# Optimization experiments

Hardware: AMD Instinct MI355X
Metric: run time of the kernel (lower is better)

Reference implementation:

```python
import jax, jax.numpy as jnp
import numpy as np

BUFFER_C = 1.25

def setup_inputs() -> dict:
    key = jax.random.key(0)
    k1, k2, k3 = jax.random.split(key, 3)
    T, D, E = 4096, 1024, 8
    x = jax.random.normal(k1, (T, D), dtype=jnp.float32)
    Wg = jax.random.normal(k2, (D, E), dtype=jnp.float32) / np.sqrt(D)
    bg = jnp.zeros((E,), dtype=jnp.float32)
    W = jax.random.normal(k3, (E, D, D), dtype=jnp.float32) / np.sqrt(D)
    b = jnp.zeros((E, D), dtype=jnp.float32)
    return {"x": x, "Wg": Wg, "bg": bg, "W": W, "b": b}


def reference(x, Wg, bg, W, b):
    # Top-1 (Switch-style) routing with capacity buffer, per-expert Linear,
    # prob-weighted combine, plus load-balancing aux loss.
    T, D = x.shape
    E = W.shape[0]
    capacity = int(BUFFER_C * T / E)

    logits = x @ Wg + bg                      # [T, E]
    probs = jax.nn.softmax(logits, axis=-1)   # [T, E]
    top_idx = jnp.argmax(probs, axis=-1)      # [T]
    top_prob = jnp.take_along_axis(probs, top_idx[:, None], axis=-1)[:, 0]

    onehot = jax.nn.one_hot(top_idx, E, dtype=x.dtype)       # [T, E]
    # 1-indexed position of each token within its expert's buffer
    pos = jnp.cumsum(onehot, axis=0) * onehot                # [T, E]
    dispatch = jnp.where((onehot > 0) & (pos <= capacity), 1.0, 0.0).astype(x.dtype)

    # dense dispatch/combine equivalent of the masked per-expert loop
    xe = jnp.einsum('te,td->etd', dispatch, x)               # [E, T, D]
    ye = jnp.einsum('etd,edf->etf', xe, W) + b[:, None, :]   # [E, T, D]
    y = jnp.einsum('te,etf->tf', dispatch, ye)               # [T, D] (0 for dropped)
    out = y * top_prob[:, None]

    # aux load-balance loss: E * sum_e f_e * P_e
    f = onehot.mean(axis=0)
    P = probs.mean(axis=0)
    aux_loss = E * jnp.sum(f * P)
    return out, aux_loss
```

## Files before the change

### kernel.cpp

```cpp
#include <hip/hip_runtime.h>
#include <hip/hip_bf16.h>
#include <cstdint>

#define T_TOK 4096
#define D_DIM 1024
#define E_EXP 8
#define CAP   640
#define NBIN  64
#define MAXDROP 3456
#define MT    10

typedef __attribute__((ext_vector_type(8))) short short8;
typedef __attribute__((ext_vector_type(4))) float f32x4;

__device__ inline unsigned short f2bf(float f) {
    uint32_t u = __float_as_uint(f);
    u += 0x7fffu + ((u >> 16) & 1u);
    return (unsigned short)(u >> 16);
}

__device__ inline void dma16(const void* g, void* l) {
    __builtin_amdgcn_global_load_lds(
        (const __attribute__((address_space(1))) unsigned int*)g,
        (__attribute__((address_space(3))) unsigned int*)l, 16, 0, 0);
}

#define WB_TILE(e, nt, kt) ((((size_t)(e) * 16 + (nt)) * 16 + (kt)) * 4096)
#define XG_TILE(e, mt, kt) ((((size_t)(e) * MT + (mt)) * 16 + (kt)) * 4096)

__global__ __launch_bounds__(256) void prep_kernel(
    const float* __restrict__ x, const float* __restrict__ Wg,
    const float* __restrict__ bg, const float* __restrict__ W,
    unsigned short* __restrict__ Wb,
    int* __restrict__ top_idx, float* __restrict__ top_prob, float* __restrict__ ppart)
{
    int bid = blockIdx.x;
    int tid = threadIdx.x;

    if (bid < 2048) {
        __shared__ unsigned short tile[64][66];
        int e  = bid >> 8;
        int kt = (bid >> 4) & 15;
        int nt = bid & 15;
        int k0 = kt * 64, n0 = nt * 64;
        const float* Wsrc = W + (size_t)e * D_DIM * D_DIM;
        #pragma unroll
        for (int p = 0; p < 4; p++) {
            int kk = p * 16 + (tid >> 4);
            int nn = (tid & 15) * 4;
            float4 v = *(const float4*)(Wsrc + (size_t)(k0 + kk) * D_DIM + n0 + nn);
            ushort4 u;
            u.x = f2bf(v.x); u.y = f2bf(v.y); u.z = f2bf(v.z); u.w = f2bf(v.w);
            *(ushort4*)&tile[kk][nn] = u;
        }
        __syncthreads();
        unsigned short* dst = Wb + WB_TILE(e, nt, kt);
        #pragma unroll
        for (int p = 0; p < 2; p++) {
            int c = tid + 256 * p;
            int g = c >> 6, n = c & 63;
            short8 v;
            #pragma unroll
            for (int z = 0; z < 8; z++) v[z] = (short)tile[g * 8 + z][n];
            *(short8*)&dst[(size_t)c * 8] = v;
        }
    } else {
        int wid  = tid >> 6;
        int lane = tid & 63;
        int t = (bid - 2048) * 4 + wid;

        const float* xr = x + (size_t)t * D_DIM;

        float acc[8];
        #pragma unroll
        for (int e = 0; e < 8; e++) acc[e] = 0.f;

        #pragma unroll
        for (int ii = 0; ii < 16; ii++) {
            int d = lane + 64 * ii;
            float xv = xr[d];
            const float4* wr = (const float4*)(Wg + (size_t)d * 8);
            float4 a = wr[0], bq = wr[1];
            acc[0] += xv * a.x;  acc[1] += xv * a.y;
            acc[2] += xv * a.z;  acc[3] += xv * a.w;
            acc[4] += xv * bq.x; acc[5] += xv * bq.y;
            acc[6] += xv * bq.z; acc[7] += xv * bq.w;
        }
        #pragma unroll
        for (int off = 32; off > 0; off >>= 1) {
            #pragma unroll
            for (int e = 0; e < 8; e++) acc[e] += __shfl_xor(acc[e], off, 64);
        }
        if (lane == 0) {
            float lg[8];
            #pragma unroll
            for (int e = 0; e < 8; e++) lg[e] = acc[e] + bg[e];
            float m = lg[0]; int am = 0;
            #pragma unroll
            for (int e = 1; e < 8; e++) { if (lg[e] > m) { m = lg[e]; am = e; } }
            float ex[8], s = 0.f;
            #pragma unroll
            for (int e = 0; e < 8; e++) { ex[e] = expf(lg[e] - m); s += ex[e]; }
            float inv = 1.f / s;
            top_idx[t]  = am;
            top_prob[t] = ex[am] * inv;
            int bin = (int)(bid & (NBIN - 1));
            #pragma unroll
            for (int e = 0; e < 8; e++) atomicAdd(&ppart[bin * 8 + e], ex[e] * inv);
        }
    }
}

__global__ __launch_bounds__(1024) void scan_kernel(
    const int* __restrict__ top_idx,
    int* __restrict__ tok_list, int* __restrict__ cnt,
    const float* __restrict__ ppart,
    float* __restrict__ out, float* __restrict__ out_aux)
{
    __shared__ int counts[64][8];
    __shared__ int excl[64][8];
    __shared__ int fulltot[8];
    __shared__ int droplist[MAXDROP];
    __shared__ int ndrop;

    int tid  = threadIdx.x;
    int wv   = tid >> 6;
    int lane = tid & 63;
    unsigned long long ltmask = (lane == 0) ? 0ull : ((~0ull) >> (64 - lane));

    if (tid == 0) ndrop = 0;

    int ecache[4];
    #pragma unroll
    for (int c = 0; c < 4; c++)
        ecache[c] = top_idx[(4 * wv + c) * 64 + lane];

    #pragma unroll
    for (int c = 0; c < 4; c++) {
        int chunk = 4 * wv + c;
        int e = ecache[c];
        #pragma unroll
        for (int q = 0; q < 8; q++) {
            unsigned long long mk = __ballot(e == q);
            int tot = __popcll(mk);
            if (lane == q) counts[chunk][q] = tot;
        }
    }
    __syncthreads();

    if (wv == 0) {
        #pragma unroll
        for (int q = 0; q < 8; q++) {
            int v = counts[lane][q];
            int orig = v;
            #pragma unroll
            for (int off = 1; off < 64; off <<= 1) {
                int n = __shfl_up(v, off, 64);
                if (lane >= off) v += n;
            }
            excl[lane][q] = v - orig;
            int total = __shfl(v, 63, 64);
            if (lane == 0) {
                fulltot[q] = total;
                cnt[q] = total < CAP ? total : CAP;
            }
        }
    }
    __syncthreads();

    #pragma unroll
    for (int c = 0; c < 4; c++) {
        int chunk = 4 * wv + c;
        int t = chunk * 64 + lane;
        int e = ecache[c];
        int pos = 0;
        #pragma unroll
        for (int q = 0; q < 8; q++) {
            unsigned long long mk = __ballot(e == q);
            if (e == q) pos = excl[chunk][q] + __popcll(mk & ltmask);
        }
        if (pos < CAP) {
            tok_list[e * CAP + pos] = t;
        } else {
            int di = atomicAdd(&ndrop, 1);
            droplist[di] = t;
        }
    }
    __syncthreads();

    int nd = ndrop;
    int grp = tid >> 8;
    int col = (tid & 255) * 4;
    float4 z = {0.f, 0.f, 0.f, 0.f};
    for (int d = grp; d < nd; d += 4) {
        int row = droplist[d];
        *(float4*)&out[(size_t)row * D_DIM + col] = z;
    }

    if (wv == 0) {
        float p[8];
        #pragma unroll
        for (int e = 0; e < 8; e++) p[e] = ppart[lane * 8 + e];
        #pragma unroll
        for (int off = 32; off > 0; off >>= 1) {
            #pragma unroll
            for (int e = 0; e < 8; e++) p[e] += __shfl_xor(p[e], off, 64);
        }
        if (lane == 0) {
            float s = 0.f;
            #pragma unroll
            for (int e = 0; e < 8; e++)
                s += ((float)fulltot[e] / (float)T_TOK) * (p[e] / (float)T_TOK);
            out_aux[0] = (float)E_EXP * s;
        }
    }
}

__global__ __launch_bounds__(256) void gather_kernel(
    const float* __restrict__ x, const int* __restrict__ tok_list,
    const int* __restrict__ cnt, unsigned short* __restrict__ xg)
{
    int bid = blockIdx.x;
    int e   = bid / 40;
    int rem = bid % 40;
    int mt  = rem >> 2, ktg = rem & 3;
    int count = cnt[e];
    int m0 = mt * 64;
    if (m0 >= count) return;

    int tid = threadIdx.x;
    const int* tl = tok_list + e * CAP;

    #pragma unroll
    for (int kk = 0; kk < 4; kk++) {
        int kt = ktg * 4 + kk;
        unsigned short* dst = xg + XG_TILE(e, mt, kt);
        #pragma unroll
        for (int p = 0; p < 2; p++) {
            int c = tid + 256 * p;
            int g = c >> 6, row = c & 63;
            int gm = m0 + row;
            int tok = tl[gm < count ? gm : count - 1];
            const float* src = x + (size_t)tok * D_DIM + kt * 64 + g * 8;
            float4 v0 = *(const float4*)(src);
            float4 v1 = *(const float4*)(src + 4);
            short8 v;
            v[0] = f2bf(v0.x); v[1] = f2bf(v0.y); v[2] = f2bf(v0.z); v[3] = f2bf(v0.w);
            v[4] = f2bf(v1.x); v[5] = f2bf(v1.y); v[6] = f2bf(v1.z); v[7] = f2bf(v1.w);
            *(short8*)&dst[(size_t)c * 8] = v;
        }
    }
}

__device__ inline void stage_dma(const unsigned short* gAt, const unsigned short* gBt,
                                 unsigned short (*Ab)[64][8], unsigned short (*Bb)[64][8],
                                 int w, int lane)
{
    size_t lo = (size_t)lane * 8;
    dma16(gAt + (size_t)w * 512 + lo,       &Ab[w][0][0]);
    dma16(gAt + (size_t)(w + 4) * 512 + lo, &Ab[w + 4][0][0]);
    dma16(gBt + (size_t)w * 512 + lo,       &Bb[w][0][0]);
    dma16(gBt + (size_t)(w + 4) * 512 + lo, &Bb[w + 4][0][0]);
}

__global__ __launch_bounds__(256) void expert_gemm(
    const unsigned short* __restrict__ xg, const unsigned short* __restrict__ Wb,
    const float* __restrict__ bias,
    const int* __restrict__ tok_list, const int* __restrict__ cnt,
    const float* __restrict__ top_prob, float* __restrict__ out)
{
    int bid = blockIdx.x;
    int e   = bid / (MT * 16);
    int rem = bid % (MT * 16);
    int mt  = rem >> 4, nt = rem & 15;
    int count = cnt[e];
    int m0 = mt * 64;
    if (m0 >= count) return;
    int n0 = nt * 64;

    __shared__ unsigned short Ab[2][8][64][8];
    __shared__ unsigned short Bb[2][8][64][8];

    int tid  = threadIdx.x;
    int lane = tid & 63, w = tid >> 6;
    int quad = lane >> 4, l16 = lane & 15;
    int mw = (w >> 1) * 32, nw = (w & 1) * 32;

    const int* tl = tok_list + e * CAP;
    const unsigned short* gA0 = xg + XG_TILE(e, mt, 0);
    const unsigned short* gB0 = Wb + WB_TILE(e, nt, 0);

    f32x4 acc[2][2];
    #pragma unroll
    for (int i = 0; i < 2; i++)
        #pragma unroll
        for (int j = 0; j < 2; j++)
            acc[i][j] = (f32x4){0.f, 0.f, 0.f, 0.f};

    stage_dma(gA0, gB0, Ab[0], Bb[0], w, lane);

    int cur = 0;
    #pragma unroll 1
    for (int kt = 0; kt < 16; kt++) {
        __syncthreads();
        if (kt + 1 < 16)
            stage_dma(gA0 + (size_t)(kt + 1) * 4096, gB0 + (size_t)(kt + 1) * 4096,
                      Ab[cur ^ 1], Bb[cur ^ 1], w, lane);

        short8 af[2][2], bf[2][2];
        #pragma unroll
        for (int s = 0; s < 2; s++) {
            #pragma unroll
            for (int i = 0; i < 2; i++) {
                af[s][i] = *(const short8*)&Ab[cur][s * 4 + quad][mw + 16 * i + l16][0];
                bf[s][i] = *(const short8*)&Bb[cur][s * 4 + quad][nw + 16 * i + l16][0];
            }
        }
        #pragma unroll
        for (int s = 0; s < 2; s++)
            #pragma unroll
            for (int i = 0; i < 2; i++)
                #pragma unroll
                for (int j = 0; j < 2; j++)
                    acc[i][j] = __builtin_amdgcn_mfma_f32_16x16x32_bf16(
                        af[s][i], bf[s][j], acc[i][j], 0, 0, 0);
        cur ^= 1;
    }

    float bv[2];
    #pragma unroll
    for (int j = 0; j < 2; j++)
        bv[j] = bias[e * D_DIM + n0 + nw + 16 * j + l16];

    #pragma unroll
    for (int i = 0; i < 2; i++) {
        int rb = m0 + mw + 16 * i + quad * 4;
        #pragma unroll
        for (int r = 0; r < 4; r++) {
            int gm = rb + r;
            if (gm >= count) continue;
            int tok = tl[gm];
            float p = top_prob[tok];
            float* orow = out + (size_t)tok * D_DIM + n0 + nw + l16;
            #pragma unroll
            for (int j = 0; j < 2; j++)
                orow[16 * j] = (acc[i][j][r] + bv[j]) * p;
        }
    }
}

extern "C" void kernel_launch(void* const* d_in, const int* in_sizes, int n_in,
                              void* d_out, int out_size, void* d_ws, size_t ws_size,
                              hipStream_t stream) {
    const float* x  = (const float*)d_in[0];
    const float* Wg = (const float*)d_in[1];
    const float* bg = (const float*)d_in[2];
    const float* W  = (const float*)d_in[3];
    const float* b  = (const float*)d_in[4];
    float* out = (float*)d_out;

    char* ws = (char*)d_ws;
    unsigned short* Wb = (unsigned short*)(ws + 0);
    unsigned short* xg = (unsigned short*)(ws + 16777216);
    int*   top_idx  = (int*)(ws + 27262976);
    float* top_prob = (float*)(ws + 27279360);
    int*   tok_list = (int*)(ws + 27295744);
    int*   cnt      = (int*)(ws + 27316224);
    float* ppart    = (float*)(ws + 27316256);

    hipMemsetAsync(ppart, 0, NBIN * 8 * sizeof(float), stream);
    hipLaunchKernelGGL(prep_kernel, dim3(2048 + T_TOK / 4), dim3(256), 0, stream,
                       x, Wg, bg, W, Wb, top_idx, top_prob, ppart);
    hipLaunchKernelGGL(scan_kernel, dim3(1), dim3(1024), 0, stream,
                       top_idx, tok_list, cnt, ppart, out, out + (size_t)T_TOK * D_DIM);
    hipLaunchKernelGGL(gather_kernel, dim3(320), dim3(256), 0, stream,
                       x, tok_list, cnt, xg);
    hipLaunchKernelGGL(expert_gemm, dim3(E_EXP * MT * 16), dim3(256), 0, stream,
                       xg, Wb, b, tok_list, cnt, top_prob, out);
}
```

Before: 170.2 us.

## Replace atomic prob accumulation with per-block partials and widen gather grid

The router blocks now write per-block probability sums through shared memory instead of doing global atomicAdds into binned accumulators, and the scan kernel reduces the 1024 partials across all its waves. This removes the memset launch and the atomic contention. The gating blocks are moved ahead of the weight-conversion blocks so routing finishes earlier. The gather kernel also uses one block per k-tile instead of four, giving 4x more blocks for better parallelism, and expf is swapped for __expf, which can slightly change the softmax values.

```diff
diff --git a/kernel.cpp b/kernel.cpp
--- a/kernel.cpp
+++ b/kernel.cpp
@@ -6,9 +6,9 @@
 #define D_DIM 1024
 #define E_EXP 8
 #define CAP   640
-#define NBIN  64
 #define MAXDROP 3456
 #define MT    10
+#define GBLK  1024
 
 typedef __attribute__((ext_vector_type(8))) short short8;
 typedef __attribute__((ext_vector_type(4))) float f32x4;
@@ -32,16 +32,18 @@
     const float* __restrict__ x, const float* __restrict__ Wg,
     const float* __restrict__ bg, const float* __restrict__ W,
     unsigned short* __restrict__ Wb,
-    int* __restrict__ top_idx, float* __restrict__ top_prob, float* __restrict__ ppart)
+    int* __restrict__ top_idx, float* __restrict__ top_prob,
+    float* __restrict__ blkpart)
 {
     int bid = blockIdx.x;
     int tid = threadIdx.x;
 
-    if (bid < 2048) {
+    if (bid >= GBLK) {
         __shared__ unsigned short tile[64][66];
-        int e  = bid >> 8;
-        int kt = (bid >> 4) & 15;
-        int nt = bid & 15;
+        int bid2 = bid - GBLK;
+        int e  = bid2 >> 8;
+        int kt = (bid2 >> 4) & 15;
+        int nt = bid2 & 15;
         int k0 = kt * 64, n0 = nt * 64;
         const float* Wsrc = W + (size_t)e * D_DIM * D_DIM;
         #pragma unroll
@@ -65,9 +67,10 @@
             *(short8*)&dst[(size_t)c * 8] = v;
         }
     } else {
+        __shared__ float probs_sm[4][8];
         int wid  = tid >> 6;
         int lane = tid & 63;
-        int t = (bid - 2048) * 4 + wid;
+        int t = bid * 4 + wid;
 
         const float* xr = x + (size_t)t * D_DIM;
 
@@ -100,13 +103,20 @@
             for (int e = 1; e < 8; e++) { if (lg[e] > m) { m = lg[e]; am = e; } }
             float ex[8], s = 0.f;
             #pragma unroll
-            for (int e = 0; e < 8; e++) { ex[e] = expf(lg[e] - m); s += ex[e]; }
+            for (int e = 0; e < 8; e++) { ex[e] = __expf(lg[e] - m); s += ex[e]; }
             float inv = 1.f / s;
             top_idx[t]  = am;
             top_prob[t] = ex[am] * inv;
-            int bin = (int)(bid & (NBIN - 1));
-            #pragma unroll
-            for (int e = 0; e < 8; e++) atomicAdd(&ppart[bin * 8 + e], ex[e] * inv);
+            #pragma unroll
+            for (int e = 0; e < 8; e++) probs_sm[wid][e] = 0.f;
+            #pragma unroll
+            for (int e = 0; e < 8; e++) probs_sm[wid][e] = ex[e] * inv;
+        }
+        __syncthreads();
+        if (tid < 8) {
+            float s = probs_sm[0][tid] + probs_sm[1][tid]
+                    + probs_sm[2][tid] + probs_sm[3][tid];
+            blkpart[(size_t)bid * 8 + tid] = s;
         }
     }
 }
@@ -114,7 +124,7 @@
 __global__ __launch_bounds__(1024) void scan_kernel(
     const int* __restrict__ top_idx,
     int* __restrict__ tok_list, int* __restrict__ cnt,
-    const float* __restrict__ ppart,
+    const float* __restrict__ blkpart,
     float* __restrict__ out, float* __restrict__ out_aux)
 {
     __shared__ int counts[64][8];
@@ -122,6 +132,7 @@
     __shared__ int fulltot[8];
     __shared__ int droplist[MAXDROP];
     __shared__ int ndrop;
+    __shared__ float wpart[16][8];
 
     int tid  = threadIdx.x;
     int wv   = tid >> 6;
@@ -129,6 +140,14 @@
     unsigned long long ltmask = (lane == 0) ? 0ull : ((~0ull) >> (64 - lane));
 
     if (tid == 0) ndrop = 0;
+
+    float p[8];
+    {
+        const float4* bp = (const float4*)(blkpart + (size_t)tid * 8);
+        float4 p0 = bp[0], p1 = bp[1];
+        p[0] = p0.x; p[1] = p0.y; p[2] = p0.z; p[3] = p0.w;
+        p[4] = p1.x; p[5] = p1.y; p[6] = p1.z; p[7] = p1.w;
+    }
 
     int ecache[4];
     #pragma unroll
@@ -186,6 +205,16 @@
             droplist[di] = t;
         }
     }
+
+    #pragma unroll
+    for (int off = 32; off > 0; off >>= 1) {
+        #pragma unroll
+        for (int e = 0; e < 8; e++) p[e] += __shfl_xor(p[e], off, 64);
+    }
+    if (lane == 0) {
+        #pragma unroll
+        for (int e = 0; e < 8; e++) wpart[wv][e] = p[e];
+    }
     __syncthreads();
 
     int nd = ndrop;
@@ -197,22 +226,16 @@
         *(float4*)&out[(size_t)row * D_DIM + col] = z;
     }
 
-    if (wv == 0) {
-        float p[8];
-        #pragma unroll
-        for (int e = 0; e < 8; e++) p[e] = ppart[lane * 8 + e];
-        #pragma unroll
-        for (int off = 32; off > 0; off >>= 1) {
-            #pragma unroll
-            for (int e = 0; e < 8; e++) p[e] += __shfl_xor(p[e], off, 64);
-        }
-        if (lane == 0) {
-            float s = 0.f;
-            #pragma unroll
-            for (int e = 0; e < 8; e++)
-                s += ((float)fulltot[e] / (float)T_TOK) * (p[e] / (float)T_TOK);
-            out_aux[0] = (float)E_EXP * s;
-        }
+    if (tid == 0) {
+        float s = 0.f;
+        #pragma unroll
+        for (int e = 0; e < 8; e++) {
+            float Pe = 0.f;
+            #pragma unroll
+            for (int w = 0; w < 16; w++) Pe += wpart[w][e];
+            s += ((float)fulltot[e] / (float)T_TOK) * (Pe / (float)T_TOK);
+        }
+        out_aux[0] = (float)E_EXP * s;
     }
 }
 
@@ -221,34 +244,30 @@
     const int* __restrict__ cnt, unsigned short* __restrict__ xg)
 {
     int bid = blockIdx.x;
-    int e   = bid / 40;
-    int rem = bid % 40;
-    int mt  = rem >> 2, ktg = rem & 3;
+    int e   = bid / (MT * 16);
+    int rem = bid % (MT * 16);
+    int mt  = rem >> 4, kt = rem & 15;
     int count = cnt[e];
     int m0 = mt * 64;
     if (m0 >= count) return;
 
     int tid = threadIdx.x;
     const int* tl = tok_list + e * CAP;
-
-    #pragma unroll
-    for (int kk = 0; kk < 4; kk++) {
-        int kt = ktg * 4 + kk;
-        unsigned short* dst = xg + XG_TILE(e, mt, kt);
-        #pragma unroll
-        for (int p = 0; p < 2; p++) {
-            int c = tid + 256 * p;
-            int g = c >> 6, row = c & 63;
-            int gm = m0 + row;
-            int tok = tl[gm < count ? gm : count - 1];
-            const float* src = x + (size_t)tok * D_DIM + kt * 64 + g * 8;
-            float4 v0 = *(const float4*)(src);
-            float4 v1 = *(const float4*)(src + 4);
-            short8 v;
-            v[0] = f2bf(v0.x); v[1] = f2bf(v0.y); v[2] = f2bf(v0.z); v[3] = f2bf(v0.w);
-            v[4] = f2bf(v1.x); v[5] = f2bf(v1.y); v[6] = f2bf(v1.z); v[7] = f2bf(v1.w);
-            *(short8*)&dst[(size_t)c * 8] = v;
-        }
+    unsigned short* dst = xg + XG_TILE(e, mt, kt);
+
+    #pragma unroll
+    for (int p = 0; p < 2; p++) {
+        int c = tid + 256 * p;
+        int g = c >> 6, row = c & 63;
+        int gm = m0 + row;
+        int tok = tl[gm < count ? gm : count - 1];
+        const float* src = x + (size_t)tok * D_DIM + kt * 64 + g * 8;
+        float4 v0 = *(const float4*)(src);
+        float4 v1 = *(const float4*)(src + 4);
+        short8 v;
+        v[0] = f2bf(v0.x); v[1] = f2bf(v0.y); v[2] = f2bf(v0.z); v[3] = f2bf(v0.w);
+        v[4] = f2bf(v1.x); v[5] = f2bf(v1.y); v[6] = f2bf(v1.z); v[7] = f2bf(v1.w);
+        *(short8*)&dst[(size_t)c * 8] = v;
     }
 }
 
@@ -366,14 +385,13 @@
     float* top_prob = (float*)(ws + 27279360);
     int*   tok_list = (int*)(ws + 27295744);
     int*   cnt      = (int*)(ws + 27316224);
-    float* ppart    = (float*)(ws + 27316256);
-
-    hipMemsetAsync(ppart, 0, NBIN * 8 * sizeof(float), stream);
-    hipLaunchKernelGGL(prep_kernel, dim3(2048 + T_TOK / 4), dim3(256), 0, stream,
-                       x, Wg, bg, W, Wb, top_idx, top_prob, ppart);
+    float* blkpart  = (float*)(ws + 27316256);
+
+    hipLaunchKernelGGL(prep_kernel, dim3(GBLK + 2048), dim3(256), 0, stream,
+                       x, Wg, bg, W, Wb, top_idx, top_prob, blkpart);
     hipLaunchKernelGGL(scan_kernel, dim3(1), dim3(1024), 0, stream,
-                       top_idx, tok_list, cnt, ppart, out, out + (size_t)T_TOK * D_DIM);
-    hipLaunchKernelGGL(gather_kernel, dim3(320), dim3(256), 0, stream,
+                       top_idx, tok_list, cnt, blkpart, out, out + (size_t)T_TOK * D_DIM);
+    hipLaunchKernelGGL(gather_kernel, dim3(E_EXP * MT * 16), dim3(256), 0, stream,
                        x, tok_list, cnt, xg);
     hipLaunchKernelGGL(expert_gemm, dim3(E_EXP * MT * 16), dim3(256), 0, stream,
                        xg, Wb, b, tok_list, cnt, top_prob, out);
```

After: 143.3 us. -15.8%, faster.
